# Kernel tuning notes

Measured on AMD Instinct MI355X. Metric: run time of the kernel, lower is better.

## Reference

```python
import jax, jax.numpy as jnp
import numpy as np

ALPHA, BETA, GAMMA = 1.0, 0.5, 0.3
EPS = 1e-08


def setup_inputs() -> dict:
    key = jax.random.key(0)
    k1, k2, k3, k4, k5 = jax.random.split(key, 5)
    B, C, F = 32, 256, 2048
    return {
        "mag_hat": jax.random.normal(k1, (B, C, F), dtype=jnp.float32),
        "phase_hat": jax.random.normal(k2, (B, C, F), dtype=jnp.float32),
        "mag_target": jax.random.normal(k3, (B, C, F), dtype=jnp.float32),
        "phase_target": jax.random.normal(k4, (B, C, F), dtype=jnp.float32),
        "pci_target": jax.random.uniform(k5, (B, C, C), dtype=jnp.float32),
    }


def _pci(phase):
    # phase: (B, C, F). Naive form is mean_f cos/sin(phi_i - phi_j) over a
    # (B,C,C,F) broadcast; rewrite with cos(a-b)=ca*cb+sa*sb and
    # sin(a-b)=sa*cb-ca*sb as two batched GEMMs on (C,F) matrices.
    c = jnp.cos(phase)
    s = jnp.sin(phase)
    inv_f = 1.0 / phase.shape[-1]
    real = (jnp.einsum('bif,bjf->bij', c, c) + jnp.einsum('bif,bjf->bij', s, s)) * inv_f
    imag = (jnp.einsum('bif,bjf->bij', s, c) - jnp.einsum('bif,bjf->bij', c, s)) * inv_f
    return jnp.sqrt(real * real + imag * imag + EPS)


def reference(mag_hat, phase_hat, mag_target, phase_target, pci_target):
    mag_loss = jnp.mean((mag_hat - mag_target) ** 2)
    phase_loss = jnp.mean(1.0 - jnp.cos(phase_hat - phase_target))
    pci_hat = _pci(phase_hat)
    coh_loss = jnp.mean((pci_hat - pci_target) ** 2)
    total = ALPHA * mag_loss + BETA * phase_loss + GAMMA * coh_loss
    return (total, mag_loss, phase_loss, coh_loss)
```

## Files before the change

kernel.cpp:

```cpp
#include <hip/hip_runtime.h>
#include <hip/hip_bf16.h>

#define ALPHA_ 1.0f
#define BETA_  0.5f
#define GAMMA_ 0.3f
#define EPS_   1e-8f

typedef unsigned short u16;
typedef unsigned int u32;

constexpr int B_ = 32, C_ = 256, F_ = 2048;
constexpr int NTOT = B_ * C_ * F_;
constexpr int G8   = NTOT / 8;
constexpr int NCC  = B_ * C_ * C_;

typedef __bf16 bf16x8 __attribute__((ext_vector_type(8)));
typedef float  f32x4  __attribute__((ext_vector_type(4)));

__device__ __forceinline__ u32 f2bf(float x) {
    unsigned u = __float_as_uint(x);
    u += 0x7fffu + ((u >> 16) & 1u);
    return (u >> 16);
}

__device__ __forceinline__ void async_copy16(const void* g, void* l) {
    __builtin_amdgcn_global_load_lds(
        (const __attribute__((address_space(1))) unsigned int*)g,
        (__attribute__((address_space(3))) unsigned int*)l,
        16, 0, 0);
}

__device__ __forceinline__ void ew_body(int g,
    float4 p0, float4 p1, float4 q0, float4 q1,
    float4 a0, float4 a1, float4 b0, float4 b1,
    float& msum, float& psum, int4* __restrict__ cb4, int4* __restrict__ sb4)
{
    float pv[8] = {p0.x, p0.y, p0.z, p0.w, p1.x, p1.y, p1.z, p1.w};
    float qv[8] = {q0.x, q0.y, q0.z, q0.w, q1.x, q1.y, q1.z, q1.w};
    float av[8] = {a0.x, a0.y, a0.z, a0.w, a1.x, a1.y, a1.z, a1.w};
    float bv[8] = {b0.x, b0.y, b0.z, b0.w, b1.x, b1.y, b1.z, b1.w};
    u32 cu[8], su[8];
    #pragma unroll
    for (int j = 0; j < 8; j++) {
        float dm = av[j] - bv[j];
        msum += dm * dm;
        psum += 1.f - __cosf(pv[j] - qv[j]);
        float s, c;
        __sincosf(pv[j], &s, &c);
        cu[j] = f2bf(c);
        su[j] = f2bf(s);
    }
    cb4[g] = make_int4((int)(cu[0] | (cu[1] << 16)), (int)(cu[2] | (cu[3] << 16)),
                       (int)(cu[4] | (cu[5] << 16)), (int)(cu[6] | (cu[7] << 16)));
    sb4[g] = make_int4((int)(su[0] | (su[1] << 16)), (int)(su[2] | (su[3] << 16)),
                       (int)(su[4] | (su[5] << 16)), (int)(su[6] | (su[7] << 16)));
}

__global__ void __launch_bounds__(256)
ew_kernel(const float4* __restrict__ mh, const float4* __restrict__ ph,
          const float4* __restrict__ mt, const float4* __restrict__ pt,
          int4* __restrict__ cb4, int4* __restrict__ sb4,
          float* __restrict__ accum)
{
    __shared__ float sm[4], sp[4];
    const int tid    = blockIdx.x * 256 + threadIdx.x;
    const int stride = 2048 * 256;
    float msum = 0.f, psum = 0.f;

    #pragma unroll
    for (int half = 0; half < 2; ++half) {
        int g0 = tid + (2 * half) * stride;
        int g1 = g0 + stride;
        float4 p00 = ph[2*g0], p01 = ph[2*g0+1];
        float4 q00 = pt[2*g0], q01 = pt[2*g0+1];
        float4 a00 = mh[2*g0], a01 = mh[2*g0+1];
        float4 b00 = mt[2*g0], b01 = mt[2*g0+1];
        float4 p10 = ph[2*g1], p11 = ph[2*g1+1];
        float4 q10 = pt[2*g1], q11 = pt[2*g1+1];
        float4 a10 = mh[2*g1], a11 = mh[2*g1+1];
        float4 b10 = mt[2*g1], b11 = mt[2*g1+1];
        ew_body(g0, p00, p01, q00, q01, a00, a01, b00, b01, msum, psum, cb4, sb4);
        ew_body(g1, p10, p11, q10, q11, a10, a11, b10, b11, msum, psum, cb4, sb4);
    }

    #pragma unroll
    for (int o = 32; o > 0; o >>= 1) {
        msum += __shfl_down(msum, o, 64);
        psum += __shfl_down(psum, o, 64);
    }
    int lane = threadIdx.x & 63, wv = threadIdx.x >> 6;
    if (lane == 0) { sm[wv] = msum; sp[wv] = psum; }
    __syncthreads();
    if (threadIdx.x == 0) {
        atomicAdd(&accum[0], sm[0] + sm[1] + sm[2] + sm[3]);
        atomicAdd(&accum[1], sp[0] + sp[1] + sp[2] + sp[3]);
    }
}

__global__ void __launch_bounds__(256)
pci_kernel(const u16* __restrict__ cb, const u16* __restrict__ sb,
           const float* __restrict__ tgt, float* __restrict__ accum)
{
    __shared__ char lds[32768];
    __shared__ float sred[4];
    char* la = lds;
    char* lb = lds + 16384;

    const int g  = blockIdx.x;
    const int x  = g & 7, sq = g >> 3;
    const int y  = (x << 2) | (sq & 3);
    const int tt = sq >> 2;
    const int i0 = (tt >> 2) * 64, j0 = (tt & 3) * 64;

    const int t    = threadIdx.x;
    const int lane = t & 63, w = t >> 6;
    const int wrow = (w >> 1) * 32, wcol = (w & 1) * 32;
    const int m = lane & 15, q = lane >> 4;

    const char* gA[4];
    const char* gB[4];
    {
        const int p = lane & 15;
        #pragma unroll
        for (int r = 0; r < 4; ++r) {
            int row = w * 16 + r * 4 + (lane >> 4);
            int c   = p ^ (row & 15);
            const u16* arr = (c < 8) ? cb : sb;
            int cc = c & 7;
            gA[r] = (const char*)arr + ((size_t)(y * 256 + i0 + row)) * 4096 + cc * 16;
            gB[r] = (const char*)arr + ((size_t)(y * 256 + j0 + row)) * 4096 + cc * 16;
        }
    }

    f32x4 zero = {0.f, 0.f, 0.f, 0.f};
    f32x4 accR[2][2], accSC[2][2], accCS[2][2];
    #pragma unroll
    for (int a = 0; a < 2; a++)
        #pragma unroll
        for (int c = 0; c < 2; c++) {
            accR[a][c] = zero; accSC[a][c] = zero; accCS[a][c] = zero;
        }

    for (int it = 0; it < 32; ++it) {
        __syncthreads();
        #pragma unroll
        for (int r = 0; r < 4; ++r) {
            async_copy16(gA[r], la + w * 4096 + r * 1024);
            async_copy16(gB[r], lb + w * 4096 + r * 1024);
            gA[r] += 128; gB[r] += 128;
        }
        __syncthreads();

        #pragma unroll
        for (int s = 0; s < 2; ++s) {
            bf16x8 fac[2], fas[2], fbc[2], fbs[2];
            #pragma unroll
            for (int a = 0; a < 2; a++) {
                const char* base = la + (wrow + a * 16 + m) * 256;
                int pc = ((4 * s + q) ^ m) * 16;
                fac[a] = *(const bf16x8*)(base + pc);
                fas[a] = *(const bf16x8*)(base + (pc ^ 128));
            }
            #pragma unroll
            for (int c = 0; c < 2; c++) {
                const char* base = lb + (wcol + c * 16 + m) * 256;
                int pc = ((4 * s + q) ^ m) * 16;
                fbc[c] = *(const bf16x8*)(base + pc);
                fbs[c] = *(const bf16x8*)(base + (pc ^ 128));
            }
            #pragma unroll
            for (int a = 0; a < 2; a++)
                #pragma unroll
                for (int c = 0; c < 2; c++) {
                    accR[a][c]  = __builtin_amdgcn_mfma_f32_16x16x32_bf16(fac[a], fbc[c], accR[a][c], 0, 0, 0);
                    accR[a][c]  = __builtin_amdgcn_mfma_f32_16x16x32_bf16(fas[a], fbs[c], accR[a][c], 0, 0, 0);
                    accSC[a][c] = __builtin_amdgcn_mfma_f32_16x16x32_bf16(fas[a], fbc[c], accSC[a][c], 0, 0, 0);
                    accCS[a][c] = __builtin_amdgcn_mfma_f32_16x16x32_bf16(fac[a], fbs[c], accCS[a][c], 0, 0, 0);
                }
        }
    }

    const float inv_f = 1.0f / (float)F_;
    float coh = 0.f;
    const float* tb = tgt + (size_t)y * (C_ * C_);
    #pragma unroll
    for (int a = 0; a < 2; a++)
        #pragma unroll
        for (int c = 0; c < 2; c++) {
            int irow = i0 + wrow + a * 16 + q * 4;
            int jcol = j0 + wcol + c * 16 + m;
            #pragma unroll
            for (int r = 0; r < 4; r++) {
                float re = accR[a][c][r] * inv_f;
                float im = (accSC[a][c][r] - accCS[a][c][r]) * inv_f;
                float p  = sqrtf(re * re + im * im + EPS_);
                float d  = p - tb[(irow + r) * C_ + jcol];
                coh += d * d;
            }
        }

    #pragma unroll
    for (int o = 32; o > 0; o >>= 1) coh += __shfl_down(coh, o, 64);
    if (lane == 0) sred[w] = coh;
    __syncthreads();
    if (t == 0) atomicAdd(&accum[2], sred[0] + sred[1] + sred[2] + sred[3]);
}

__global__ void fin_kernel(const float* __restrict__ accum, float* __restrict__ out)
{
    if (threadIdx.x == 0) {
        float mag = accum[0] * (1.0f / (float)NTOT);
        float phs = accum[1] * (1.0f / (float)NTOT);
        float coh = accum[2] * (1.0f / (float)NCC);
        out[0] = ALPHA_ * mag + BETA_ * phs + GAMMA_ * coh;
        out[1] = mag;
        out[2] = phs;
        out[3] = coh;
    }
}

extern "C" void kernel_launch(void* const* d_in, const int* in_sizes, int n_in,
                              void* d_out, int out_size, void* d_ws, size_t ws_size,
                              hipStream_t stream)
{
    const float* mh  = (const float*)d_in[0];
    const float* ph  = (const float*)d_in[1];
    const float* mt  = (const float*)d_in[2];
    const float* pt  = (const float*)d_in[3];
    const float* tgt = (const float*)d_in[4];
    float* out = (float*)d_out;

    float* accum = (float*)d_ws;
    u16* cb = (u16*)((char*)d_ws + 256);
    u16* sb = cb + (size_t)NTOT;

    hipMemsetAsync(d_ws, 0, 16, stream);

    ew_kernel<<<2048, 256, 0, stream>>>(
        (const float4*)mh, (const float4*)ph, (const float4*)mt, (const float4*)pt,
        (int4*)cb, (int4*)sb, accum);

    pci_kernel<<<512, 256, 0, stream>>>(cb, sb, tgt, accum);

    fin_kernel<<<1, 64, 0, stream>>>(accum, out);
}
```

Before: 308.4 us.

## Exploit PCI symmetry and split-K the Gram GEMM with atomic reduction

The PCI magnitude matrix is symmetric, so the GEMM now computes only the 10 upper-triangular 64x64 tiles per batch instead of 16. Each tile's F reduction is also split four ways across blocks, which reaches 1280 blocks and gives better occupancy. Partial re and im sums are accumulated with float atomics into a workspace buffer that a memset clears first. A new coh_kernel applies the sqrt and target comparison, counting each off-diagonal tile against both the target and its transpose. The cost is the extra memset, one extra kernel launch, atomic traffic on the partial buffers, and strided transposed reads of the target.

Result: slower. 320.9 us (+4.1%).

```diff
diff --git a/kernel.cpp b/kernel.cpp
--- a/kernel.cpp
+++ b/kernel.cpp
@@ -13,6 +13,13 @@
 constexpr int NTOT = B_ * C_ * F_;
 constexpr int G8   = NTOT / 8;
 constexpr int NCC  = B_ * C_ * C_;
+constexpr int NPOS = 10;
+constexpr int KSPL = 4;
+constexpr int NBLK = B_ * NPOS * KSPL;
+constexpr int NRED = B_ * NPOS * 64 * 64;
+
+__constant__ int TI_[NPOS] = {0, 1, 2, 3, 0, 0, 0, 1, 1, 2};
+__constant__ int TJ_[NPOS] = {0, 1, 2, 3, 1, 2, 3, 2, 3, 3};
 
 typedef __bf16 bf16x8 __attribute__((ext_vector_type(8)));
 typedef float  f32x4  __attribute__((ext_vector_type(4)));
@@ -56,7 +63,7 @@
                        (int)(su[4] | (su[5] << 16)), (int)(su[6] | (su[7] << 16)));
 }
 
-__global__ void __launch_bounds__(256)
+__global__ void __launch_bounds__(256, 4)
 ew_kernel(const float4* __restrict__ mh, const float4* __restrict__ ph,
           const float4* __restrict__ mt, const float4* __restrict__ pt,
           int4* __restrict__ cb4, int4* __restrict__ sb4,
@@ -99,18 +106,19 @@
 
 __global__ void __launch_bounds__(256)
 pci_kernel(const u16* __restrict__ cb, const u16* __restrict__ sb,
-           const float* __restrict__ tgt, float* __restrict__ accum)
+           float* __restrict__ reb, float* __restrict__ imb)
 {
     __shared__ char lds[32768];
-    __shared__ float sred[4];
     char* la = lds;
     char* lb = lds + 16384;
 
-    const int g  = blockIdx.x;
-    const int x  = g & 7, sq = g >> 3;
-    const int y  = (x << 2) | (sq & 3);
-    const int tt = sq >> 2;
-    const int i0 = (tt >> 2) * 64, j0 = (tt & 3) * 64;
+    const int bid = blockIdx.x;
+    const int l   = (bid & 7) * (NBLK / 8) + (bid >> 3);
+    const int h   = l & 3;
+    const int t4  = l >> 2;
+    const int pos = t4 % NPOS;
+    const int y   = t4 / NPOS;
+    const int i0 = TI_[pos] * 64, j0 = TJ_[pos] * 64;
 
     const int t    = threadIdx.x;
     const int lane = t & 63, w = t >> 6;
@@ -127,8 +135,8 @@
             int c   = p ^ (row & 15);
             const u16* arr = (c < 8) ? cb : sb;
             int cc = c & 7;
-            gA[r] = (const char*)arr + ((size_t)(y * 256 + i0 + row)) * 4096 + cc * 16;
-            gB[r] = (const char*)arr + ((size_t)(y * 256 + j0 + row)) * 4096 + cc * 16;
+            gA[r] = (const char*)arr + ((size_t)(y * 256 + i0 + row)) * 4096 + cc * 16 + h * 1024;
+            gB[r] = (const char*)arr + ((size_t)(y * 256 + j0 + row)) * 4096 + cc * 16 + h * 1024;
         }
     }
 
@@ -141,7 +149,7 @@
             accR[a][c] = zero; accSC[a][c] = zero; accCS[a][c] = zero;
         }
 
-    for (int it = 0; it < 32; ++it) {
+    for (int it = 0; it < 8; ++it) {
         __syncthreads();
         #pragma unroll
         for (int r = 0; r < 4; ++r) {
@@ -180,30 +188,65 @@
         }
     }
 
-    const float inv_f = 1.0f / (float)F_;
+    const int tb = (y * NPOS + pos) * 4096;
+    #pragma unroll
+    for (int a = 0; a < 2; a++)
+        #pragma unroll
+        for (int c = 0; c < 2; c++) {
+            int ii = wrow + a * 16 + q * 4;
+            int jj = wcol + c * 16 + m;
+            #pragma unroll
+            for (int r = 0; r < 4; r++) {
+                int idx = tb + (ii + r) * 64 + jj;
+                atomicAdd(&reb[idx], accR[a][c][r]);
+                atomicAdd(&imb[idx], accSC[a][c][r] - accCS[a][c][r]);
+            }
+        }
+}
+
+__global__ void __launch_bounds__(256)
+coh_kernel(const float* __restrict__ reb, const float* __restrict__ imb,
+           const float* __restrict__ tgt, float* __restrict__ accum)
+{
+    __shared__ float sred[4];
+    const int tid  = blockIdx.x * 256 + threadIdx.x;
+    const int e0   = tid * 8;
+    const int tile = e0 >> 12;
+    const int y    = tile / NPOS;
+    const int pos  = tile % NPOS;
+    const int ii   = (e0 & 4095) >> 6;
+    const int jj0  = e0 & 63;
+    const int ig   = TI_[pos] * 64 + ii;
+    const int jg   = TJ_[pos] * 64 + jj0;
+    const bool off = (pos >= 4);
+    const float invf = 1.0f / (float)F_;
+    const float* ty = tgt + (size_t)y * (C_ * C_);
+    const float* tr = ty + ig * C_ + jg;
+
+    float4 r0 = *(const float4*)(reb + e0);
+    float4 r1 = *(const float4*)(reb + e0 + 4);
+    float4 i0 = *(const float4*)(imb + e0);
+    float4 i1 = *(const float4*)(imb + e0 + 4);
+    float rv[8] = {r0.x, r0.y, r0.z, r0.w, r1.x, r1.y, r1.z, r1.w};
+    float iv[8] = {i0.x, i0.y, i0.z, i0.w, i1.x, i1.y, i1.z, i1.w};
+
     float coh = 0.f;
-    const float* tb = tgt + (size_t)y * (C_ * C_);
-    #pragma unroll
-    for (int a = 0; a < 2; a++)
-        #pragma unroll
-        for (int c = 0; c < 2; c++) {
-            int irow = i0 + wrow + a * 16 + q * 4;
-            int jcol = j0 + wcol + c * 16 + m;
-            #pragma unroll
-            for (int r = 0; r < 4; r++) {
-                float re = accR[a][c][r] * inv_f;
-                float im = (accSC[a][c][r] - accCS[a][c][r]) * inv_f;
-                float p  = sqrtf(re * re + im * im + EPS_);
-                float d  = p - tb[(irow + r) * C_ + jcol];
-                coh += d * d;
-            }
-        }
+    #pragma unroll
+    for (int j = 0; j < 8; j++) {
+        float re = rv[j] * invf, im = iv[j] * invf;
+        float p  = sqrtf(re * re + im * im + EPS_);
+        float d  = p - tr[j];
+        coh += d * d;
+        if (off) { float d2 = p - ty[(jg + j) * C_ + ig]; coh += d2 * d2; }
+    }
 
     #pragma unroll
     for (int o = 32; o > 0; o >>= 1) coh += __shfl_down(coh, o, 64);
+    int lane = threadIdx.x & 63, w = threadIdx.x >> 6;
     if (lane == 0) sred[w] = coh;
     __syncthreads();
-    if (t == 0) atomicAdd(&accum[2], sred[0] + sred[1] + sred[2] + sred[3]);
+    if (threadIdx.x == 0)
+        atomicAdd(&accum[2], sred[0] + sred[1] + sred[2] + sred[3]);
 }
 
 __global__ void fin_kernel(const float* __restrict__ accum, float* __restrict__ out)
@@ -231,16 +274,21 @@
     float* out = (float*)d_out;
 
     float* accum = (float*)d_ws;
-    u16* cb = (u16*)((char*)d_ws + 256);
-    u16* sb = cb + (size_t)NTOT;
+    u16* cb  = (u16*)((char*)d_ws + 256);
+    u16* sb  = cb + (size_t)NTOT;
+    float* reb = (float*)(sb + (size_t)NTOT);
+    float* imb = reb + NRED;
 
     hipMemsetAsync(d_ws, 0, 16, stream);
+    hipMemsetAsync(reb, 0, (size_t)NRED * 2 * sizeof(float), stream);
 
     ew_kernel<<<2048, 256, 0, stream>>>(
         (const float4*)mh, (const float4*)ph, (const float4*)mt, (const float4*)pt,
         (int4*)cb, (int4*)sb, accum);
 
-    pci_kernel<<<512, 256, 0, stream>>>(cb, sb, tgt, accum);
+    pci_kernel<<<NBLK, 256, 0, stream>>>(cb, sb, reb, imb);
+
+    coh_kernel<<<640, 256, 0, stream>>>(reb, imb, tgt, accum);
 
     fin_kernel<<<1, 64, 0, stream>>>(accum, out);
 }
```
